# Kernel optimization log

Hardware: AMD Instinct MI355X
Metric: run time of the kernel (lower is better)

Reference implementation:

```python
import jax, jax.numpy as jnp
import numpy as np

N_NODES = 50000
N_EDGES = 800000
IN_DIM = 256
HID = 32
HEADS = 8
N_CLASSES = 40
NEG_SLOPE = 0.2  # DGL GATConv default


def setup_inputs() -> dict:
    key = jax.random.key(0)
    ks = jax.random.split(key, 9)
    x = jax.random.normal(ks[0], (N_NODES, IN_DIM), dtype=jnp.float32)
    src = jax.random.randint(ks[1], (N_EDGES,), 0, N_NODES)
    dst = jax.random.randint(ks[2], (N_EDGES,), 0, N_NODES)
    s = 0.05
    W1 = jax.random.normal(ks[3], (IN_DIM, HEADS * HID), dtype=jnp.float32) * s
    al1 = jax.random.normal(ks[4], (HEADS, HID), dtype=jnp.float32) * s
    ar1 = jax.random.normal(ks[5], (HEADS, HID), dtype=jnp.float32) * s
    W2 = jax.random.normal(ks[6], (HEADS * HID, N_CLASSES), dtype=jnp.float32) * s
    al2 = jax.random.normal(ks[7], (1, N_CLASSES), dtype=jnp.float32) * s
    ar2 = jax.random.normal(ks[8], (1, N_CLASSES), dtype=jnp.float32) * s
    return {"x": x, "src": src, "dst": dst, "W1": W1, "al1": al1, "ar1": ar1,
            "W2": W2, "al2": al2, "ar2": ar2}


def gat_conv(h, src, dst, W, al, ar, heads, dout):
    # h: [N, F_in]; W: [F_in, heads*dout]; al/ar: [heads, dout]
    feat = (h @ W).reshape(-1, heads, dout)               # [N, H, D]
    el = (feat * al).sum(-1)                               # [N, H]
    er = (feat * ar).sum(-1)                               # [N, H]
    e = jax.nn.leaky_relu(el[src] + er[dst], NEG_SLOPE)    # [E, H]
    # segment softmax over incoming edges of each dst node
    emax = jax.ops.segment_max(e, dst, num_segments=N_NODES)
    emax = lax_stop(jnp.where(jnp.isfinite(emax), emax, 0.0))
    ee = jnp.exp(e - emax[dst])                            # [E, H]
    denom = jax.ops.segment_sum(ee, dst, num_segments=N_NODES)
    alpha = ee / denom[dst]                                # [E, H]
    msg = feat[src] * alpha[:, :, None]                    # [E, H, D]
    return jax.ops.segment_sum(msg, dst, num_segments=N_NODES)  # [N, H, D]


def lax_stop(v):
    return jax.lax.stop_gradient(v)


def reference(x, src, dst, W1, al1, ar1, W2, al2, ar2):
    # eval mode: feat dropout is identity
    h = gat_conv(x, src, dst, W1, al1, ar1, HEADS, HID)    # [N, 8, 32]
    h = jax.nn.relu(h.reshape(N_NODES, HEADS * HID))       # flatten(1) + relu
    h = gat_conv(h, src, dst, W2, al2, ar2, 1, N_CLASSES)  # [N, 1, C]
    h = h.mean(axis=1)                                     # [N, C]
    return jax.nn.log_softmax(h, axis=1)
```

## Files before the change

### kernel.cpp

```cpp
#include <hip/hip_runtime.h>
#include <hip/hip_bf16.h>
#include <math.h>

#define N_NODES 50000
#define N_EDGES 800000
#define IN_DIM  256
#define HID     32
#define HEADS   8
#define NCLS    40
#define NEG     0.2f
#define CAP1    128
#define CAP2    128

using short8  = __attribute__((ext_vector_type(8))) short;
using f32x4   = __attribute__((ext_vector_type(4))) float;
using floatx2 = __attribute__((ext_vector_type(2))) float;

__device__ __forceinline__ float leaky(float x) { return x >= 0.f ? x : NEG * x; }
__device__ __forceinline__ unsigned short f2b(float f) {
    unsigned int u = __float_as_uint(f);
    unsigned int r = (u + 0x7fffu + ((u >> 16) & 1u)) >> 16;
    return (unsigned short)r;
}
__device__ __forceinline__ float b2f(unsigned short h) {
    return __uint_as_float((unsigned int)h << 16);
}


__global__ void cvt_w_k(const float* __restrict__ W1, const float* __restrict__ W2,
                        unsigned short* __restrict__ BTile, unsigned short* __restrict__ W2T) {
    int n = blockIdx.x;
    int k = threadIdx.x;
    BTile[(size_t)(k >> 5) * 8192 + n * 32 + (k & 31)] = f2b(W1[k * 256 + n]);
    if (n < 48) {
        int half = k >> 7, cs = (k & 127) >> 3, ni = k & 7;
        int ck = half * 128 + ni * 16 + cs;
        W2T[n * 256 + k] = (n < 40) ? f2b(W2[ck * 40 + n]) : (unsigned short)0;
    }
}

__global__ __launch_bounds__(256) void gemm1_mfma(const float* __restrict__ A,
                                                  const unsigned short* __restrict__ BTile,
                                                  unsigned char* __restrict__ F8, int M) {
    __shared__ unsigned short Asm[2][64][40];
    __shared__ unsigned short Bsm[2][256][40];
    int t = threadIdx.x;
    int lane = t & 63, w = t >> 6;
    int wr = w >> 1, wc = w & 1;
    int m0 = blockIdx.x * 64;
    int rsub = lane & 15, koff = (lane >> 4) * 8;
    f32x4 acc[2][8] = {};

    int ar = t >> 2, ac = (t & 3) * 8;
    const float* ap = A + (size_t)(m0 + ar) * 256 + ac;
    bool aok = (m0 + ar) < M;
    const unsigned short* bp = BTile + (size_t)t * 32;

    float4 a0 = make_float4(0.f, 0.f, 0.f, 0.f), a1 = a0;
    if (aok) { a0 = *reinterpret_cast<const float4*>(ap); a1 = *reinterpret_cast<const float4*>(ap + 4); }
    uint4 b0 = *reinterpret_cast<const uint4*>(bp);
    uint4 b1 = *reinterpret_cast<const uint4*>(bp + 8);
    uint4 b2 = *reinterpret_cast<const uint4*>(bp + 16);
    uint4 b3 = *reinterpret_cast<const uint4*>(bp + 24);
    {
        short8 bb;
        bb[0] = (short)f2b(a0.x); bb[1] = (short)f2b(a0.y); bb[2] = (short)f2b(a0.z); bb[3] = (short)f2b(a0.w);
        bb[4] = (short)f2b(a1.x); bb[5] = (short)f2b(a1.y); bb[6] = (short)f2b(a1.z); bb[7] = (short)f2b(a1.w);
        *reinterpret_cast<short8*>(&Asm[0][ar][ac]) = bb;
        *reinterpret_cast<uint4*>(&Bsm[0][t][0])  = b0;
        *reinterpret_cast<uint4*>(&Bsm[0][t][8])  = b1;
        *reinterpret_cast<uint4*>(&Bsm[0][t][16]) = b2;
        *reinterpret_cast<uint4*>(&Bsm[0][t][24]) = b3;
    }
    __syncthreads();

    for (int kt = 0; kt < 8; ++kt) {
        if (kt < 7) {
            a0 = make_float4(0.f, 0.f, 0.f, 0.f); a1 = a0;
            if (aok) {
                const float* p = ap + (kt + 1) * 32;
                a0 = *reinterpret_cast<const float4*>(p);
                a1 = *reinterpret_cast<const float4*>(p + 4);
            }
            const unsigned short* nb = bp + (size_t)(kt + 1) * 8192;
            b0 = *reinterpret_cast<const uint4*>(nb);
            b1 = *reinterpret_cast<const uint4*>(nb + 8);
            b2 = *reinterpret_cast<const uint4*>(nb + 16);
            b3 = *reinterpret_cast<const uint4*>(nb + 24);
        }
        short8 a[2], b[8];
#pragma unroll
        for (int mi = 0; mi < 2; mi++)
            a[mi] = *reinterpret_cast<const short8*>(&Asm[kt & 1][wr * 32 + mi * 16 + rsub][koff]);
#pragma unroll
        for (int ni = 0; ni < 8; ni++)
            b[ni] = *reinterpret_cast<const short8*>(&Bsm[kt & 1][wc * 128 + ni * 16 + rsub][koff]);
#pragma unroll
        for (int mi = 0; mi < 2; mi++)
#pragma unroll
            for (int ni = 0; ni < 8; ni++)
                acc[mi][ni] = __builtin_amdgcn_mfma_f32_16x16x32_bf16(a[mi], b[ni], acc[mi][ni], 0, 0, 0);
        if (kt < 7) {
            int nb2 = (kt + 1) & 1;
            short8 bb;
            bb[0] = (short)f2b(a0.x); bb[1] = (short)f2b(a0.y); bb[2] = (short)f2b(a0.z); bb[3] = (short)f2b(a0.w);
            bb[4] = (short)f2b(a1.x); bb[5] = (short)f2b(a1.y); bb[6] = (short)f2b(a1.z); bb[7] = (short)f2b(a1.w);
            *reinterpret_cast<short8*>(&Asm[nb2][ar][ac]) = bb;
            *reinterpret_cast<uint4*>(&Bsm[nb2][t][0])  = b0;
            *reinterpret_cast<uint4*>(&Bsm[nb2][t][8])  = b1;
            *reinterpret_cast<uint4*>(&Bsm[nb2][t][16]) = b2;
            *reinterpret_cast<uint4*>(&Bsm[nb2][t][24]) = b3;
            __syncthreads();
        }
    }

    int rgrp = (lane >> 4) * 4, csub = lane & 15;
#pragma unroll
    for (int mi = 0; mi < 2; mi++) {
#pragma unroll
        for (int i = 0; i < 4; i++) {
            int r = m0 + wr * 32 + mi * 16 + rgrp + i;
            if (r < M) {
                int d0 = __builtin_amdgcn_cvt_pk_fp8_f32(acc[mi][0][i], acc[mi][1][i], 0, false);
                d0 = __builtin_amdgcn_cvt_pk_fp8_f32(acc[mi][2][i], acc[mi][3][i], d0, true);
                int d1 = __builtin_amdgcn_cvt_pk_fp8_f32(acc[mi][4][i], acc[mi][5][i], 0, false);
                d1 = __builtin_amdgcn_cvt_pk_fp8_f32(acc[mi][6][i], acc[mi][7][i], d1, true);
                uint2 st; st.x = (unsigned)d0; st.y = (unsigned)d1;
                *reinterpret_cast<uint2*>(F8 + (size_t)r * 256 + wc * 128 + csub * 8) = st;
            }
        }
    }
}

__global__ __launch_bounds__(256) void elr1_k(const unsigned char* __restrict__ feat8,
                                              const float* __restrict__ al,
                                              const float* __restrict__ ar,
                                              float* __restrict__ el, float* __restrict__ er) {
    int wid = (blockIdx.x * blockDim.x + threadIdx.x) >> 6;
    int lane = threadIdx.x & 63;
    if (wid >= N_NODES) return;
    unsigned u = *reinterpret_cast<const unsigned*>(feat8 + (size_t)wid * 256 + 4 * lane);
    floatx2 lo = __builtin_amdgcn_cvt_pk_f32_fp8((int)u, false);
    floatx2 hi = __builtin_amdgcn_cvt_pk_f32_fp8((int)u, true);
    int csub = (lane & 31) >> 1;
    int h0 = (lane >> 5) * 4 + 2 * (lane & 1);
    float pl0 = lo.x * al[h0 * 32 + csub] + lo.y * al[h0 * 32 + 16 + csub];
    float pr0 = lo.x * ar[h0 * 32 + csub] + lo.y * ar[h0 * 32 + 16 + csub];
    float pl1 = hi.x * al[(h0 + 1) * 32 + csub] + hi.y * al[(h0 + 1) * 32 + 16 + csub];
    float pr1 = hi.x * ar[(h0 + 1) * 32 + csub] + hi.y * ar[(h0 + 1) * 32 + 16 + csub];
#pragma unroll
    for (int d = 2; d <= 16; d <<= 1) {
        pl0 += __shfl_xor(pl0, d); pr0 += __shfl_xor(pr0, d);
        pl1 += __shfl_xor(pl1, d); pr1 += __shfl_xor(pr1, d);
    }
    if (csub == 0) {
        el[wid * 8 + h0] = pl0; el[wid * 8 + h0 + 1] = pl1;
        er[wid * 8 + h0] = pr0; er[wid * 8 + h0 + 1] = pr1;
    }
}

__global__ __launch_bounds__(256) void gemm2_mfma(const unsigned short* __restrict__ A,
                                                  const unsigned short* __restrict__ BT,
                                                  const float* __restrict__ al2,
                                                  const float* __restrict__ ar2,
                                                  unsigned short* __restrict__ C,
                                                  float* __restrict__ el2,
                                                  float* __restrict__ er2, int M) {
    __shared__ unsigned short Asm[2][64][40];
    int t = threadIdx.x;
    int lane = t & 63, w = t >> 6;
    int m0 = blockIdx.x * 64;
    int rsub = lane & 15, koff = (lane >> 4) * 8;
    f32x4 acc[3] = {};

    int r_t = t >> 2, c8 = (t & 3) * 8;
    const unsigned short* ap = A + (size_t)(m0 + r_t) * 256 + c8;
    bool arow_ok = (m0 + r_t) < M;

    uint4 s0 = make_uint4(0, 0, 0, 0);
    if (arow_ok) s0 = *reinterpret_cast<const uint4*>(ap);
    *reinterpret_cast<uint4*>(&Asm[0][r_t][c8]) = s0;
    __syncthreads();

    for (int kt = 0; kt < 8; ++kt) {
        if (kt < 7) {
            s0 = make_uint4(0, 0, 0, 0);
            if (arow_ok) s0 = *reinterpret_cast<const uint4*>(ap + (kt + 1) * 32);
        }
        short8 b[3], a;
#pragma unroll
        for (int ni = 0; ni < 3; ni++)
            b[ni] = *reinterpret_cast<const short8*>(BT + (size_t)(ni * 16 + rsub) * 256 + kt * 32 + koff);
        a = *reinterpret_cast<const short8*>(&Asm[kt & 1][w * 16 + rsub][koff]);
#pragma unroll
        for (int ni = 0; ni < 3; ni++)
            acc[ni] = __builtin_amdgcn_mfma_f32_16x16x32_bf16(a, b[ni], acc[ni], 0, 0, 0);
        if (kt < 7) {
            *reinterpret_cast<uint4*>(&Asm[(kt + 1) & 1][r_t][c8]) = s0;
            __syncthreads();
        }
    }

    int rgrp = (lane >> 4) * 4, csub = lane & 15;
    float alc[3], arc[3];
#pragma unroll
    for (int ni = 0; ni < 3; ni++) {
        int col = ni * 16 + csub;
        alc[ni] = (col < 40) ? al2[col] : 0.f;
        arc[ni] = (col < 40) ? ar2[col] : 0.f;
    }
#pragma unroll
    for (int i = 0; i < 4; i++) {
        int r = m0 + w * 16 + rgrp + i;
        float pl = acc[0][i] * alc[0] + acc[1][i] * alc[1] + acc[2][i] * alc[2];
        float pr = acc[0][i] * arc[0] + acc[1][i] * arc[1] + acc[2][i] * arc[2];
        pl += __shfl_xor(pl, 1); pl += __shfl_xor(pl, 2);
        pl += __shfl_xor(pl, 4); pl += __shfl_xor(pl, 8);
        pr += __shfl_xor(pr, 1); pr += __shfl_xor(pr, 2);
        pr += __shfl_xor(pr, 4); pr += __shfl_xor(pr, 8);
        if (r < M) {
#pragma unroll
            for (int ni = 0; ni < 3; ni++)
                C[(size_t)r * 64 + ni * 16 + csub] = f2b(acc[ni][i]);
            C[(size_t)r * 64 + 48 + csub] = 0;
            if (csub == 0) { el2[r] = pl; er2[r] = pr; }
        }
    }
}

__global__ void hist_k(const int* __restrict__ dst, int* __restrict__ deg) {
    int e4 = blockIdx.x * blockDim.x + threadIdx.x;
    if (e4 * 4 >= N_EDGES) return;
    int4 d = *reinterpret_cast<const int4*>(dst + e4 * 4);
    atomicAdd(&deg[d.x], 1);
    atomicAdd(&deg[d.y], 1);
    atomicAdd(&deg[d.z], 1);
    atomicAdd(&deg[d.w], 1);
}

__global__ void scan1_k(const int* __restrict__ deg, int* __restrict__ offs,
                        int* __restrict__ bsum, int n) {
    __shared__ int s[256];
    int tid = threadIdx.x;
    int i = blockIdx.x * 256 + tid;
    int v = (i < n) ? deg[i] : 0;
    s[tid] = v;
    __syncthreads();
    for (int d = 1; d < 256; d <<= 1) {
        int t = (tid >= d) ? s[tid - d] : 0;
        __syncthreads();
        s[tid] += t;
        __syncthreads();
    }
    if (i < n) offs[i] = s[tid] - v;
    if (tid == 255) bsum[blockIdx.x] = s[255];
}

__global__ void scan3_k(int* __restrict__ offs, const int* __restrict__ bsum,
                        int* __restrict__ cur, int n, int nb) {
    __shared__ int red[256];
    int tid = threadIdx.x;
    int v = (tid < blockIdx.x && tid < nb) ? bsum[tid] : 0;
    red[tid] = v;
    __syncthreads();
#pragma unroll
    for (int d = 128; d > 0; d >>= 1) {
        if (tid < d) red[tid] += red[tid + d];
        __syncthreads();
    }
    int prefix = red[0];
    int i = blockIdx.x * 256 + tid;
    if (i < n) { offs[i] += prefix; cur[i] = 0; }
    if (i == 0) offs[n] = N_EDGES;
}

__global__ void scatter_k(const int* __restrict__ src, const int* __restrict__ dst,
                          const int* __restrict__ offs, int* __restrict__ cur,
                          int* __restrict__ ssorted) {
    int e4 = blockIdx.x * blockDim.x + threadIdx.x;
    if (e4 * 4 >= N_EDGES) return;
    int4 d = *reinterpret_cast<const int4*>(dst + e4 * 4);
    int4 sv = *reinterpret_cast<const int4*>(src + e4 * 4);
    int p;
    p = atomicAdd(&cur[d.x], 1); ssorted[offs[d.x] + p] = sv.x;
    p = atomicAdd(&cur[d.y], 1); ssorted[offs[d.y] + p] = sv.y;
    p = atomicAdd(&cur[d.z], 1); ssorted[offs[d.z] + p] = sv.z;
    p = atomicAdd(&cur[d.w], 1); ssorted[offs[d.w] + p] = sv.w;
}

__global__ __launch_bounds__(256) void agg1_k(const unsigned char* __restrict__ feat8,
                                              const float* __restrict__ el,
                                              const float* __restrict__ er,
                                              const int* __restrict__ offs,
                                              const int* __restrict__ ssorted,
                                              unsigned short* __restrict__ h1) {
    __shared__ float sa[4][CAP1 * 8];
    __shared__ int   ss[4][CAP1];
    int t = threadIdx.x;
    int wv = t >> 6, lane = t & 63;
    int n = blockIdx.x * 4 + wv;
    if (n >= N_NODES) return;
    int beg = offs[n];
    int deg = offs[n + 1] - beg;
    int eloc = lane >> 3, h = lane & 7;
    int h0 = (lane >> 5) * 4 + 2 * (lane & 1);
    float er_h = er[n * 8 + h];

    float acc0 = 0.f, acc1 = 0.f, acc2 = 0.f, acc3 = 0.f;

    if (deg <= CAP1) {
        float ssum = 0.f;
        int c0 = 0;
        for (; c0 + 32 <= deg; c0 += 32) {
#pragma unroll
            for (int q = 0; q < 4; q++) {
                int idx = c0 + q * 8 + eloc;
                int s = ssorted[beg + idx];
                if (h == 0) ss[wv][idx] = s;
                float ee = __expf(leaky(el[s * 8 + h] + er_h));
                sa[wv][idx * 8 + h] = ee;
                ssum += ee;
            }
        }
        for (; c0 < deg; c0 += 8) {
            int idx = c0 + eloc;
            if (idx < deg) {
                int s = ssorted[beg + idx];
                if (h == 0) ss[wv][idx] = s;
                float ee = __expf(leaky(el[s * 8 + h] + er_h));
                sa[wv][idx * 8 + h] = ee;
                ssum += ee;
            }
        }
        ssum += __shfl_xor(ssum, 8);
        ssum += __shfl_xor(ssum, 16);
        ssum += __shfl_xor(ssum, 32);
        float inv = 1.f / ssum;
        float iv0 = __shfl(inv, h0), iv1 = __shfl(inv, h0 + 1);
        asm volatile("s_waitcnt lgkmcnt(0)" ::: "memory");
        for (c0 = 0; c0 < deg; c0 += 32) {
            int nr = deg - c0; if (nr > 32) nr = 32;
            unsigned u[32];
#pragma unroll
            for (int j = 0; j < 32; j++) {
                if (j < nr) {
                    int sj = ss[wv][c0 + j];
                    u[j] = *reinterpret_cast<const unsigned*>(feat8 + (size_t)sj * 256 + 4 * lane);
                }
            }
#pragma unroll
            for (int j = 0; j < 32; j++) {
                if (j < nr) {
                    float2 av = *reinterpret_cast<const float2*>(&sa[wv][(c0 + j) * 8 + h0]);
                    floatx2 lo = __builtin_amdgcn_cvt_pk_f32_fp8((int)u[j], false);
                    floatx2 hi = __builtin_amdgcn_cvt_pk_f32_fp8((int)u[j], true);
                    acc0 += av.x * lo.x;
                    acc1 += av.x * lo.y;
                    acc2 += av.y * hi.x;
                    acc3 += av.y * hi.y;
                }
            }
        }
        acc0 *= iv0; acc1 *= iv0; acc2 *= iv1; acc3 *= iv1;
    } else {
        float ssum = 0.f;
        for (int c0 = 0; c0 < deg; c0 += 8) {
            bool act = (c0 + eloc) < deg;
            float ee = 0.f;
            if (act) {
                int s = ssorted[beg + c0 + eloc];
                ee = __expf(leaky(el[s * 8 + h] + er_h));
            }
            ssum += ee;
        }
        ssum += __shfl_xor(ssum, 8);
        ssum += __shfl_xor(ssum, 16);
        ssum += __shfl_xor(ssum, 32);
        float inv = 1.f / ssum;
        float iv0 = __shfl(inv, h0), iv1 = __shfl(inv, h0 + 1);
        for (int c0 = 0; c0 < deg; c0 += 8) {
            int nr = deg - c0; if (nr > 8) nr = 8;
            int s = 0; float a = 0.f;
            if (eloc < nr) {
                s = ssorted[beg + c0 + eloc];
                a = __expf(leaky(el[s * 8 + h] + er_h));
            }
#pragma unroll
            for (int j = 0; j < 8; j++) {
                if (j < nr) {
                    int   sj = __shfl(s, j * 8);
                    float a0 = __shfl(a, j * 8 + h0) * iv0;
                    float a1 = __shfl(a, j * 8 + h0 + 1) * iv1;
                    unsigned u = *reinterpret_cast<const unsigned*>(feat8 + (size_t)sj * 256 + 4 * lane);
                    floatx2 lo = __builtin_amdgcn_cvt_pk_f32_fp8((int)u, false);
                    floatx2 hi = __builtin_amdgcn_cvt_pk_f32_fp8((int)u, true);
                    acc0 += a0 * lo.x;
                    acc1 += a0 * lo.y;
                    acc2 += a1 * hi.x;
                    acc3 += a1 * hi.y;
                }
            }
        }
    }
    ushort4 o;
    o.x = f2b(fmaxf(acc0, 0.f));
    o.y = f2b(fmaxf(acc1, 0.f));
    o.z = f2b(fmaxf(acc2, 0.f));
    o.w = f2b(fmaxf(acc3, 0.f));
    *reinterpret_cast<ushort4*>(h1 + (size_t)n * 256 + 4 * lane) = o;
}

__global__ __launch_bounds__(256) void agg2_k(const unsigned short* __restrict__ feat2p,
                                              const float* __restrict__ el2,
                                              const float* __restrict__ er2,
                                              const int* __restrict__ offs,
                                              const int* __restrict__ ssorted,
                                              float* __restrict__ out) {
    __shared__ float sa[4][CAP2];
    __shared__ int   ss[4][CAP2];
    int t = threadIdx.x;
    int wv = t >> 6, lane = t & 63;
    int n = blockIdx.x * 4 + wv;
    if (n >= N_NODES) return;
    int beg = offs[n];
    int deg = offs[n + 1] - beg;
    float ern = er2[n];
    int eloc = lane >> 3, c8 = lane & 7;

    float acc[8] = {};
    if (deg <= CAP2) {
        float ssum = 0.f;
        for (int c0 = 0; c0 < deg; c0 += 64) {
            int idx = c0 + lane;
            if (idx < deg) {
                int s = ssorted[beg + idx];
                ss[wv][idx] = s;
                float ee = __expf(leaky(el2[s] + ern));
                sa[wv][idx] = ee;
                ssum += ee;
            }
        }
#pragma unroll
        for (int d = 1; d < 64; d <<= 1) ssum += __shfl_xor(ssum, d);
        float inv = 1.f / ssum;
        asm volatile("s_waitcnt lgkmcnt(0)" ::: "memory");
        for (int c0 = 0; c0 < deg; c0 += 32) {
            uint4 v[4]; float wgt[4];
#pragma unroll
            for (int q = 0; q < 4; q++) {
                int idx = c0 + q * 8 + eloc;
                v[q] = make_uint4(0, 0, 0, 0); wgt[q] = 0.f;
                if (idx < deg) {
                    int s = ss[wv][idx]; wgt[q] = sa[wv][idx];
                    v[q] = *reinterpret_cast<const uint4*>(feat2p + (size_t)s * 64 + c8 * 8);
                }
            }
#pragma unroll
            for (int q = 0; q < 4; q++) {
                const unsigned short* pv = reinterpret_cast<const unsigned short*>(&v[q]);
#pragma unroll
                for (int i = 0; i < 8; i++) acc[i] += wgt[q] * b2f(pv[i]);
            }
        }
#pragma unroll
        for (int i = 0; i < 8; i++) acc[i] *= inv;
    } else {
        float ssum = 0.f;
        for (int c0 = 0; c0 < deg; c0 += 64) {
            bool act = (c0 + lane) < deg;
            if (act) ssum += __expf(leaky(el2[ssorted[beg + c0 + lane]] + ern));
        }
#pragma unroll
        for (int d = 1; d < 64; d <<= 1) ssum += __shfl_xor(ssum, d);
        float inv = 1.f / ssum;
        for (int c0 = 0; c0 < deg; c0 += 8) {
            int nr = deg - c0; if (nr > 8) nr = 8;
            if (eloc < nr) {
                int s = ssorted[beg + c0 + eloc];
                float a = __expf(leaky(el2[s] + ern)) * inv;
                uint4 v = *reinterpret_cast<const uint4*>(feat2p + (size_t)s * 64 + c8 * 8);
                const unsigned short* pv = reinterpret_cast<const unsigned short*>(&v);
#pragma unroll
                for (int i = 0; i < 8; i++) acc[i] += a * b2f(pv[i]);
            }
        }
    }
#pragma unroll
    for (int i = 0; i < 8; i++) {
        acc[i] += __shfl_xor(acc[i], 8);
        acc[i] += __shfl_xor(acc[i], 16);
        acc[i] += __shfl_xor(acc[i], 32);
    }
    float lmax = -INFINITY;
    if (c8 < 5) {
#pragma unroll
        for (int i = 0; i < 8; i++) lmax = fmaxf(lmax, acc[i]);
    }
    lmax = fmaxf(lmax, __shfl_xor(lmax, 1));
    lmax = fmaxf(lmax, __shfl_xor(lmax, 2));
    lmax = fmaxf(lmax, __shfl_xor(lmax, 4));
    float lsum = 0.f;
    if (c8 < 5) {
#pragma unroll
        for (int i = 0; i < 8; i++) lsum += __expf(acc[i] - lmax);
    }
    lsum += __shfl_xor(lsum, 1);
    lsum += __shfl_xor(lsum, 2);
    lsum += __shfl_xor(lsum, 4);
    if (eloc == 0 && c8 < 5) {
        float lg = __logf(lsum);
        float* o = out + (size_t)n * 40 + c8 * 8;
#pragma unroll
        for (int i = 0; i < 8; i++) o[i] = acc[i] - lmax - lg;
    }
}

extern "C" void kernel_launch(void* const* d_in, const int* in_sizes, int n_in,
                              void* d_out, int out_size, void* d_ws, size_t ws_size,
                              hipStream_t stream) {
    (void)in_sizes; (void)n_in; (void)out_size; (void)ws_size;
    const float* x   = (const float*)d_in[0];
    const int*   src = (const int*)d_in[1];
    const int*   dst = (const int*)d_in[2];
    const float* W1  = (const float*)d_in[3];
    const float* al1 = (const float*)d_in[4];
    const float* ar1 = (const float*)d_in[5];
    const float* W2  = (const float*)d_in[6];
    const float* al2 = (const float*)d_in[7];
    const float* ar2 = (const float*)d_in[8];
    float* out = (float*)d_out;

    char* ws = (char*)d_ws;
    size_t off = 0;
    auto alloc = [&](size_t bytes) {
        void* p = ws + off;
        off += (bytes + 255) & ~(size_t)255;
        return p;
    };
    unsigned short* w1tile = (unsigned short*)alloc((size_t)8 * 256 * 32 * 2);
    unsigned short* w2t    = (unsigned short*)alloc((size_t)48 * 256 * 2);
    unsigned char*  feat8  = (unsigned char*)alloc((size_t)N_NODES * 256);
    unsigned short* h1p    = (unsigned short*)alloc((size_t)N_NODES * 256 * 2);
    unsigned short* feat2p = (unsigned short*)alloc((size_t)N_NODES * 64 * 2);
    float* el1   = (float*)alloc((size_t)N_NODES * 8 * 4);
    float* er1   = (float*)alloc((size_t)N_NODES * 8 * 4);
    float* el2   = (float*)alloc((size_t)N_NODES * 4);
    float* er2   = (float*)alloc((size_t)N_NODES * 4);
    int* deg     = (int*)alloc((size_t)N_NODES * 4);
    int* offs    = (int*)alloc((size_t)(N_NODES + 1) * 4);
    int* cur     = (int*)alloc((size_t)N_NODES * 4);
    int* bsum    = (int*)alloc(1024 * 4);
    int* ssorted = (int*)alloc((size_t)N_EDGES * 4);

    hipMemsetAsync(deg, 0, (size_t)N_NODES * 4, stream);

    cvt_w_k<<<256, 256, 0, stream>>>(W1, W2, w1tile, w2t);

    hist_k<<<(N_EDGES / 4 + 255) / 256, 256, 0, stream>>>(dst, deg);
    int nb = (N_NODES + 255) / 256;
    scan1_k<<<nb, 256, 0, stream>>>(deg, offs, bsum, N_NODES);
    scan3_k<<<nb, 256, 0, stream>>>(offs, bsum, cur, N_NODES, nb);
    scatter_k<<<(N_EDGES / 4 + 255) / 256, 256, 0, stream>>>(src, dst, offs, cur, ssorted);

    gemm1_mfma<<<(N_NODES + 63) / 64, 256, 0, stream>>>(x, w1tile, feat8, N_NODES);
    elr1_k<<<(N_NODES * 64 + 255) / 256, 256, 0, stream>>>(feat8, al1, ar1, el1, er1);
    agg1_k<<<(N_NODES + 3) / 4, 256, 0, stream>>>(feat8, el1, er1, offs, ssorted, h1p);

    gemm2_mfma<<<(N_NODES + 63) / 64, 256, 0, stream>>>(h1p, w2t, al2, ar2, feat2p, el2, er2, N_NODES);
    agg2_k<<<(N_NODES + 3) / 4, 256, 0, stream>>>(feat2p, el2, er2, offs, ssorted, out);
}
```

Measured before the change: 217.5 us.

## Merge weight conversion with histogram, compact layer-2 features, batch gathers in agg1

Weight conversion and the degree histogram now run in one launch, which saves a kernel launch. Layer-2 features are stored compactly with 40 columns instead of padded to 64, so the gathers in agg2 move less data, and the fifth lane group skips loading. In agg1, the index and el loads are batched ahead of the exp computations, with an extra 16-edge loop for the remainder. The feature gather batch grows from 32 to 48 to raise memory-level parallelism, at the cost of more registers and possibly lower occupancy. Rows of 40 bf16 are 80 bytes, so the uint4 loads stay 16-byte aligned.

```diff
diff --git a/kernel.cpp b/kernel.cpp
--- a/kernel.cpp
+++ b/kernel.cpp
@@ -27,15 +27,25 @@
 }
 
 
-__global__ void cvt_w_k(const float* __restrict__ W1, const float* __restrict__ W2,
-                        unsigned short* __restrict__ BTile, unsigned short* __restrict__ W2T) {
-    int n = blockIdx.x;
-    int k = threadIdx.x;
-    BTile[(size_t)(k >> 5) * 8192 + n * 32 + (k & 31)] = f2b(W1[k * 256 + n]);
-    if (n < 48) {
-        int half = k >> 7, cs = (k & 127) >> 3, ni = k & 7;
-        int ck = half * 128 + ni * 16 + cs;
-        W2T[n * 256 + k] = (n < 40) ? f2b(W2[ck * 40 + n]) : (unsigned short)0;
+__global__ void cvt_hist_k(const float* __restrict__ W1, const float* __restrict__ W2,
+                           unsigned short* __restrict__ BTile, unsigned short* __restrict__ W2T,
+                           const int* __restrict__ dst, int* __restrict__ deg) {
+    if (blockIdx.x < 256) {
+        int n = blockIdx.x, k = threadIdx.x;
+        BTile[(size_t)(k >> 5) * 8192 + n * 32 + (k & 31)] = f2b(W1[k * 256 + n]);
+        if (n < 48) {
+            int half = k >> 7, cs = (k & 127) >> 3, ni = k & 7;
+            int ck = half * 128 + ni * 16 + cs;
+            W2T[n * 256 + k] = (n < 40) ? f2b(W2[ck * 40 + n]) : (unsigned short)0;
+        }
+    } else {
+        int e4 = (blockIdx.x - 256) * 256 + threadIdx.x;
+        if (e4 * 4 >= N_EDGES) return;
+        int4 d = *reinterpret_cast<const int4*>(dst + e4 * 4);
+        atomicAdd(&deg[d.x], 1);
+        atomicAdd(&deg[d.y], 1);
+        atomicAdd(&deg[d.z], 1);
+        atomicAdd(&deg[d.w], 1);
     }
 }
 
@@ -220,22 +230,13 @@
         pr += __shfl_xor(pr, 4); pr += __shfl_xor(pr, 8);
         if (r < M) {
 #pragma unroll
-            for (int ni = 0; ni < 3; ni++)
-                C[(size_t)r * 64 + ni * 16 + csub] = f2b(acc[ni][i]);
-            C[(size_t)r * 64 + 48 + csub] = 0;
+            for (int ni = 0; ni < 3; ni++) {
+                int col = ni * 16 + csub;
+                if (col < 40) C[(size_t)r * 40 + col] = f2b(acc[ni][i]);
+            }
             if (csub == 0) { el2[r] = pl; er2[r] = pr; }
         }
     }
-}
-
-__global__ void hist_k(const int* __restrict__ dst, int* __restrict__ deg) {
-    int e4 = blockIdx.x * blockDim.x + threadIdx.x;
-    if (e4 * 4 >= N_EDGES) return;
-    int4 d = *reinterpret_cast<const int4*>(dst + e4 * 4);
-    atomicAdd(&deg[d.x], 1);
-    atomicAdd(&deg[d.y], 1);
-    atomicAdd(&deg[d.z], 1);
-    atomicAdd(&deg[d.w], 1);
 }
 
 __global__ void scan1_k(const int* __restrict__ deg, int* __restrict__ offs,
@@ -312,12 +313,31 @@
         float ssum = 0.f;
         int c0 = 0;
         for (; c0 + 32 <= deg; c0 += 32) {
+            int s[4]; float e[4];
+#pragma unroll
+            for (int q = 0; q < 4; q++) s[q] = ssorted[beg + c0 + q * 8 + eloc];
+#pragma unroll
+            for (int q = 0; q < 4; q++) e[q] = el[s[q] * 8 + h];
 #pragma unroll
             for (int q = 0; q < 4; q++) {
                 int idx = c0 + q * 8 + eloc;
-                int s = ssorted[beg + idx];
-                if (h == 0) ss[wv][idx] = s;
-                float ee = __expf(leaky(el[s * 8 + h] + er_h));
+                if (h == 0) ss[wv][idx] = s[q];
+                float ee = __expf(leaky(e[q] + er_h));
+                sa[wv][idx * 8 + h] = ee;
+                ssum += ee;
+            }
+        }
+        for (; c0 + 16 <= deg; c0 += 16) {
+            int s[2]; float e[2];
+#pragma unroll
+            for (int q = 0; q < 2; q++) s[q] = ssorted[beg + c0 + q * 8 + eloc];
+#pragma unroll
+            for (int q = 0; q < 2; q++) e[q] = el[s[q] * 8 + h];
+#pragma unroll
+            for (int q = 0; q < 2; q++) {
+                int idx = c0 + q * 8 + eloc;
+                if (h == 0) ss[wv][idx] = s[q];
+                float ee = __expf(leaky(e[q] + er_h));
                 sa[wv][idx * 8 + h] = ee;
                 ssum += ee;
             }
@@ -338,18 +358,18 @@
         float inv = 1.f / ssum;
         float iv0 = __shfl(inv, h0), iv1 = __shfl(inv, h0 + 1);
         asm volatile("s_waitcnt lgkmcnt(0)" ::: "memory");
-        for (c0 = 0; c0 < deg; c0 += 32) {
-            int nr = deg - c0; if (nr > 32) nr = 32;
-            unsigned u[32];
-#pragma unroll
-            for (int j = 0; j < 32; j++) {
+        for (c0 = 0; c0 < deg; c0 += 48) {
+            int nr = deg - c0; if (nr > 48) nr = 48;
+            unsigned u[48];
+#pragma unroll
+            for (int j = 0; j < 48; j++) {
                 if (j < nr) {
                     int sj = ss[wv][c0 + j];
                     u[j] = *reinterpret_cast<const unsigned*>(feat8 + (size_t)sj * 256 + 4 * lane);
                 }
             }
 #pragma unroll
-            for (int j = 0; j < 32; j++) {
+            for (int j = 0; j < 48; j++) {
                 if (j < nr) {
                     float2 av = *reinterpret_cast<const float2*>(&sa[wv][(c0 + j) * 8 + h0]);
                     floatx2 lo = __builtin_amdgcn_cvt_pk_f32_fp8((int)u[j], false);
@@ -410,7 +430,7 @@
     *reinterpret_cast<ushort4*>(h1 + (size_t)n * 256 + 4 * lane) = o;
 }
 
-__global__ __launch_bounds__(256) void agg2_k(const unsigned short* __restrict__ feat2p,
+__global__ __launch_bounds__(256) void agg2_k(const unsigned short* __restrict__ feat2q,
                                               const float* __restrict__ el2,
                                               const float* __restrict__ er2,
                                               const int* __restrict__ offs,
@@ -450,9 +470,9 @@
             for (int q = 0; q < 4; q++) {
                 int idx = c0 + q * 8 + eloc;
                 v[q] = make_uint4(0, 0, 0, 0); wgt[q] = 0.f;
-                if (idx < deg) {
+                if (c8 < 5 && idx < deg) {
                     int s = ss[wv][idx]; wgt[q] = sa[wv][idx];
-                    v[q] = *reinterpret_cast<const uint4*>(feat2p + (size_t)s * 64 + c8 * 8);
+                    v[q] = *reinterpret_cast<const uint4*>(feat2q + (size_t)s * 40 + c8 * 8);
                 }
             }
 #pragma unroll
@@ -475,10 +495,10 @@
         float inv = 1.f / ssum;
         for (int c0 = 0; c0 < deg; c0 += 8) {
             int nr = deg - c0; if (nr > 8) nr = 8;
-            if (eloc < nr) {
+            if (eloc < nr && c8 < 5) {
                 int s = ssorted[beg + c0 + eloc];
                 float a = __expf(leaky(el2[s] + ern)) * inv;
-                uint4 v = *reinterpret_cast<const uint4*>(feat2p + (size_t)s * 64 + c8 * 8);
+                uint4 v = *reinterpret_cast<const uint4*>(feat2q + (size_t)s * 40 + c8 * 8);
                 const unsigned short* pv = reinterpret_cast<const unsigned short*>(&v);
 #pragma unroll
                 for (int i = 0; i < 8; i++) acc[i] += a * b2f(pv[i]);
@@ -541,7 +561,7 @@
     unsigned short* w2t    = (unsigned short*)alloc((size_t)48 * 256 * 2);
     unsigned char*  feat8  = (unsigned char*)alloc((size_t)N_NODES * 256);
     unsigned short* h1p    = (unsigned short*)alloc((size_t)N_NODES * 256 * 2);
-    unsigned short* feat2p = (unsigned short*)alloc((size_t)N_NODES * 64 * 2);
+    unsigned short* feat2q = (unsigned short*)alloc((size_t)N_NODES * 40 * 2);
     float* el1   = (float*)alloc((size_t)N_NODES * 8 * 4);
     float* er1   = (float*)alloc((size_t)N_NODES * 8 * 4);
     float* el2   = (float*)alloc((size_t)N_NODES * 4);
@@ -554,9 +574,7 @@
 
     hipMemsetAsync(deg, 0, (size_t)N_NODES * 4, stream);
 
-    cvt_w_k<<<256, 256, 0, stream>>>(W1, W2, w1tile, w2t);
-
-    hist_k<<<(N_EDGES / 4 + 255) / 256, 256, 0, stream>>>(dst, deg);
+    cvt_hist_k<<<256 + (N_EDGES / 4 + 255) / 256, 256, 0, stream>>>(W1, W2, w1tile, w2t, dst, deg);
     int nb = (N_NODES + 255) / 256;
     scan1_k<<<nb, 256, 0, stream>>>(deg, offs, bsum, N_NODES);
     scan3_k<<<nb, 256, 0, stream>>>(offs, bsum, cur, N_NODES, nb);
@@ -566,6 +584,6 @@
     elr1_k<<<(N_NODES * 64 + 255) / 256, 256, 0, stream>>>(feat8, al1, ar1, el1, er1);
     agg1_k<<<(N_NODES + 3) / 4, 256, 0, stream>>>(feat8, el1, er1, offs, ssorted, h1p);
 
-    gemm2_mfma<<<(N_NODES + 63) / 64, 256, 0, stream>>>(h1p, w2t, al2, ar2, feat2p, el2, er2, N_NODES);
-    agg2_k<<<(N_NODES + 3) / 4, 256, 0, stream>>>(feat2p, el2, er2, offs, ssorted, out);
-}
+    gemm2_mfma<<<(N_NODES + 63) / 64, 256, 0, stream>>>(h1p, w2t, al2, ar2, feat2q, el2, er2, N_NODES);
+    agg2_k<<<(N_NODES + 3) / 4, 256, 0, stream>>>(feat2q, el2, er2, offs, ssorted, out);
+}
```

Result: slower. 224.0 us (+3.0%).
